# Performance work log

Measured on AMD Instinct MI355X. Metric: run time of the kernel, lower is better.

## Reference

```python
import jax, jax.numpy as jnp
import numpy as np

B, N, D = 64, 1024, 512
H, LD = 8, 64            # num_heads, linear_hidden_dim (H*LD == D)
HIDDEN = 4 * D           # ffn_multiply = 4.0
NB = 128                 # number of timestamp buckets
EPS = 1e-6
TS_SCALE = NB / 14.0     # log1p(1e6) ~ 13.8 -> buckets span [0, NB]


def rms_norm(x, eps=EPS):
    return x * jax.lax.rsqrt(jnp.mean(x * x, axis=-1, keepdims=True) + eps)


def setup_inputs() -> dict:
    key = jax.random.key(0)
    ks = jax.random.split(key, 8)
    lengths = np.linspace(256, N, B).astype(np.int64)
    x_offsets = jnp.asarray(np.concatenate([[0], np.cumsum(lengths)]), dtype=jnp.int64)
    T = int(lengths.sum())
    x = jax.random.normal(ks[0], (T, D), dtype=jnp.float32)
    all_timestamps = jnp.sort(jax.random.randint(ks[1], (B, N), 0, 10**6, dtype=jnp.int64), axis=1)
    invalid_attn_mask = jnp.tril(jnp.ones((N, N), jnp.float32))  # causal
    uv = jax.random.normal(ks[2], (D, 3 * H * LD), dtype=jnp.float32) * 0.02
    pos_w = jax.random.normal(ks[3], (2 * N - 1,), dtype=jnp.float32) * 0.02
    ts_w = jax.random.normal(ks[4], (NB + 1,), dtype=jnp.float32) * 0.02
    w_ams = jax.random.normal(ks[5], (2 * H * LD, D), dtype=jnp.float32) * 0.02
    w1 = jax.random.normal(ks[6], (D, HIDDEN), dtype=jnp.float32) * 0.02
    w2 = jax.random.normal(ks[7], (HIDDEN, D), dtype=jnp.float32) * 0.02
    return {"x": x, "x_offsets": x_offsets, "all_timestamps": all_timestamps,
            "invalid_attn_mask": invalid_attn_mask, "uv": uv, "pos_w": pos_w,
            "ts_w": ts_w, "w_ams": w_ams, "w1": w1, "w2": w2}


def reference(x, x_offsets, all_timestamps, invalid_attn_mask, uv, pos_w, ts_w, w_ams, w1, w2):
    T = x.shape[0]
    # RMSNorm (no learned scale, matches F.rms_norm with no weight) + fused proj + SiLU
    proj = jax.nn.silu(rms_norm(x) @ uv)                       # [T, 3*H*LD]
    u, v = proj[:, :2 * H * LD], proj[:, 2 * H * LD:]          # [T,2HD'], [T,HD']
    # jagged -> padded dense
    tok = jnp.arange(T)
    seg = jnp.searchsorted(x_offsets, tok, side="right") - 1   # batch id per token
    pos = tok - x_offsets[seg]                                  # position within sequence
    padded_v = jnp.zeros((B, N, H * LD), v.dtype).at[seg, pos].set(v).reshape(B, N, H, LD)
    # positional relative bias (batch-independent)
    rel = jnp.arange(N)[:, None] - jnp.arange(N)[None, :]
    pos_attn = pos_w[rel + N - 1] * invalid_attn_mask           # [N,N]
    # temporal relative bias: log-bucketized |t_i - t_j|
    dt = jnp.abs(all_timestamps[:, :, None] - all_timestamps[:, None, :]).astype(jnp.float32)
    bucket = jnp.clip(jnp.floor(jnp.log1p(dt) * TS_SCALE), 0, NB).astype(jnp.int32)
    ts_attn = ts_w[bucket] * invalid_attn_mask[None]            # [B,N,N]
    # two-stream bias 'attention' (no softmax)
    out_pos = jnp.einsum("nm,bmhd->bnhd", pos_attn, padded_v)
    out_ts = jnp.einsum("bnm,bmhd->bnhd", ts_attn, padded_v)
    combined = jnp.concatenate([out_pos, out_ts], axis=-1).reshape(B, N, 2 * H * LD)
    attn_out = combined[seg, pos]                               # dense -> jagged, [T, 2*H*LD]
    # gated norm + multistage FFN with residuals
    ams = u * rms_norm(attn_out)
    h = x + ams @ w_ams
    out = h + jax.nn.silu(rms_norm(h) @ w1) @ w2
    return out
```

## Files before the change

### kernel.cpp

```cpp
#include <hip/hip_runtime.h>
#include <cmath>


using u16 = unsigned short;

typedef __bf16 bf16x8 __attribute__((ext_vector_type(8)));
typedef float  f32x4  __attribute__((ext_vector_type(4)));

#define TS_SCALE_F (float)(128.0 / 14.0)

__device__ __forceinline__ u16 f2b(float f) {
  unsigned u = __float_as_uint(f);
  unsigned r = 0x7FFFu + ((u >> 16) & 1u);
  return (u16)((u + r) >> 16);
}
__device__ __forceinline__ float b2f(u16 v) {
  return __uint_as_float(((unsigned)v) << 16);
}
__device__ __forceinline__ bf16x8 as_frag(uint4 r) {
  union { uint4 u; bf16x8 v; } c; c.u = r; return c.v;
}

__device__ __forceinline__ size_t ts_base_elems(int b, int nt) {
  return (size_t)b * 589824 + (size_t)(nt * (nt + 1) / 2) * 16384;
}

#define EPI_SILU_BF16 0
#define EPI_ADD_F32   1

template <int EPI>
__global__ __launch_bounds__(256, 2) void gemm_bf16(
    const u16* __restrict__ A, const u16* __restrict__ W,
    void* __restrict__ C, const float* __restrict__ ADD,
    int M, int N, int K)
{
  __shared__ u16 lA[128 * 40];
  __shared__ u16 lB[4096];

  const int tid  = threadIdx.x;
  const int t0   = blockIdx.x * 128;
  const int c0   = blockIdx.y * 128;
  const int wave = tid >> 6, lane = tid & 63;
  const int wr   = (wave >> 1) * 64, wc = (wave & 1) * 64;
  const int l15  = lane & 15, l4 = lane >> 4;

  f32x4 z = {0.f, 0.f, 0.f, 0.f};
  f32x4 acc[4][4];
#pragma unroll
  for (int m = 0; m < 4; ++m)
#pragma unroll
    for (int j = 0; j < 4; ++j) acc[m][j] = z;

  const int ar = tid >> 1, ak = (tid & 1) * 16;
  const int bk = tid >> 3, bc = (tid & 7) * 16;
  const bool arow_ok = (t0 + ar) < M;
  const u16* aptr = A + (size_t)(t0 + ar) * K + ak;
  const u16* wptr = W + (size_t)bk * N + c0 + bc;

  for (int k0 = 0; k0 < K; k0 += 32) {
    uint4 a0 = make_uint4(0, 0, 0, 0), a1 = a0;
    if (arow_ok) {
      a0 = *(const uint4*)(aptr + k0);
      a1 = *(const uint4*)(aptr + k0 + 8);
    }
    uint4 w0 = *(const uint4*)(wptr + (size_t)k0 * N);
    uint4 w1v = *(const uint4*)(wptr + (size_t)k0 * N + 8);

    *(uint4*)&lA[ar * 40 + ak]     = a0;
    *(uint4*)&lA[ar * 40 + ak + 8] = a1;
    {
      u16 tmp[16];
      *(uint4*)tmp       = w0;
      *(uint4*)(tmp + 8) = w1v;
      const int kb = bk >> 3, ke = bk & 7;
      char* base = (char*)lB;
#pragma unroll
      for (int i = 0; i < 16; ++i) {
        int col = bc + i;
        int off = (kb * 2048 + col * 16 + ke * 2) ^ (((col >> 3) & 7) << 4);
        *(u16*)(base + off) = tmp[i];
      }
    }
    __syncthreads();

    bf16x8 af[4], bfv[4];
#pragma unroll
    for (int m = 0; m < 4; ++m)
      af[m] = as_frag(*(const uint4*)&lA[(wr + m * 16 + l15) * 40 + l4 * 8]);
#pragma unroll
    for (int j = 0; j < 4; ++j) {
      int col = wc + j * 16 + l15;
      int off = (l4 * 2048 + col * 16) ^ (((col >> 3) & 7) << 4);
      bfv[j] = as_frag(*(const uint4*)((char*)lB + off));
    }
#pragma unroll
    for (int m = 0; m < 4; ++m)
#pragma unroll
      for (int j = 0; j < 4; ++j)
        acc[m][j] = __builtin_amdgcn_mfma_f32_16x16x32_bf16(af[m], bfv[j], acc[m][j], 0, 0, 0);
    __syncthreads();
  }

#pragma unroll
  for (int m = 0; m < 4; ++m) {
#pragma unroll
    for (int r = 0; r < 4; ++r) {
      int row = t0 + wr + m * 16 + l4 * 4 + r;
      if (row >= M) continue;
#pragma unroll
      for (int j = 0; j < 4; ++j) {
        int col = c0 + wc + j * 16 + l15;
        size_t idx = (size_t)row * N + col;
        float y = acc[m][j][r];
        if constexpr (EPI == EPI_SILU_BF16) {
          float s = y / (1.f + __expf(-y));
          ((u16*)C)[idx] = f2b(s);
        } else {
          ((float*)C)[idx] = y + ADD[idx];
        }
      }
    }
  }
}

__global__ __launch_bounds__(128) void pos_scores(
    const float* __restrict__ pos_w, u16* __restrict__ pos_s)
{
  const int n = blockIdx.x;
  const int m0 = threadIdx.x * 8;
  u16 o[8];
#pragma unroll
  for (int i = 0; i < 8; ++i) {
    int m = m0 + i;
    float v = (m <= n) ? pos_w[n - m + 1023] : 0.f;
    o[i] = f2b(v);
  }
  *(uint4*)(pos_s + (size_t)n * 1024 + m0) = *(uint4*)o;
}

__global__ __launch_bounds__(256) void ts_scores(
    const int* __restrict__ tstamp, const float* __restrict__ ts_w,
    u16* __restrict__ ts_s)
{
  const int nt = 7 - (blockIdx.x >> 6);
  const int b  = blockIdx.x & 63;
  const int W  = 128 * (nt + 1);
  const int n0 = nt * 128;
  const int tid = threadIdx.x;

  __shared__ float tsw[132];
  __shared__ int   tsm[1024];
  if (tid < 129) tsw[tid] = ts_w[tid];
  for (int i = tid; i < W; i += 256) tsm[i] = tstamp[b * 1024 + i];
  __syncthreads();

  const int r = tid >> 1, h = tid & 1;
  const int n_abs = n0 + r;
  const int t_n = tstamp[b * 1024 + n_abs];
  u16* row = ts_s + ts_base_elems(b, nt) + (size_t)r * W + h * (W >> 1);
  const int c0 = h * (W >> 1);
  const int half = W >> 1;

  for (int c = 0; c < half; c += 8) {
    u16 o[8];
#pragma unroll
    for (int i = 0; i < 8; ++i) {
      int m = c0 + c + i;
      int d = t_n - tsm[m];
      if (d < 0) d = -d;
      float dt = (float)d;
      int bkt = (int)(log1pf(dt) * TS_SCALE_F);
      bkt = bkt > 128 ? 128 : bkt;
      float v = (m <= n_abs) ? tsw[bkt] : 0.f;
      o[i] = f2b(v);
    }
    *(uint4*)(row + c) = *(uint4*)o;
  }
}

__global__ __launch_bounds__(256, 1) void attn_gemm(
    const u16* __restrict__ proj,
    const int* __restrict__ xoff,
    const u16* __restrict__ pos_s,
    const u16* __restrict__ ts_s,
    u16* __restrict__ attn_out,
    int Ttot)
{
  const int flat = blockIdx.x;
  const int nt = 7 - (flat >> 8);
  const int rem = flat & 255;
  const int b  = rem >> 2;
  const int ct = rem & 3;

  const int off = xoff[b];
  int len = xoff[b + 1] - off;
  if (len < 0) len = 0;
  if (len > 1024) len = 1024;
  if (off < 0 || off + len > Ttot) return;
  const int n0 = nt * 128;
  if (n0 >= len) return;
  const int c0 = ct * 128;
  const int W = 128 * (nt + 1);

  __shared__ u16 lP[128 * 40];
  __shared__ u16 lT[128 * 40];
  __shared__ u16 sV[4096];

  const int tid = threadIdx.x;
  const int wave = tid >> 6, lane = tid & 63;
  const int wr = (wave >> 1) * 64, wc = (wave & 1) * 64;
  const int l15 = lane & 15, l4 = lane >> 4;

  f32x4 z = {0.f, 0.f, 0.f, 0.f};
  f32x4 accP[4][4], accT[4][4];
#pragma unroll
  for (int m = 0; m < 4; ++m)
#pragma unroll
    for (int j = 0; j < 4; ++j) { accP[m][j] = z; accT[m][j] = z; }

  const int ar = tid >> 1, ak = (tid & 1) * 16;
  const u16* pRow = pos_s + (size_t)(n0 + ar) * 1024 + ak;
  const u16* tRow = ts_s + ts_base_elems(b, nt) + (size_t)ar * W + ak;
  const int vk = tid >> 3, vc = (tid & 7) * 16;

  const int mEnd = (n0 + 128 < len) ? (n0 + 128) : len;

  for (int m0 = 0; m0 < mEnd; m0 += 32) {
    {
      int mm = m0 + vk;
      uint4 v0 = make_uint4(0, 0, 0, 0), v1 = v0;
      if (mm < len) {
        const u16* src = proj + (size_t)(off + mm) * 1536 + 1024 + c0 + vc;
        v0 = *(const uint4*)src;
        v1 = *(const uint4*)(src + 8);
      }
      u16 tmp[16];
      *(uint4*)tmp       = v0;
      *(uint4*)(tmp + 8) = v1;
      const int kb = vk >> 3, ke = vk & 7;
#pragma unroll
      for (int i = 0; i < 16; ++i) {
        int col = vc + i;
        int o2 = (kb * 2048 + col * 16 + ke * 2) ^ (((col >> 3) & 7) << 4);
        *(u16*)((char*)sV + o2) = tmp[i];
      }
    }
    {
      uint4 p0 = *(const uint4*)(pRow + m0);
      uint4 p1 = *(const uint4*)(pRow + m0 + 8);
      uint4 t0v = *(const uint4*)(tRow + m0);
      uint4 t1v = *(const uint4*)(tRow + m0 + 8);
      int wb = ar * 40 + ak;
      *(uint4*)&lP[wb]     = p0;
      *(uint4*)&lP[wb + 8] = p1;
      *(uint4*)&lT[wb]     = t0v;
      *(uint4*)&lT[wb + 8] = t1v;
    }
    __syncthreads();

    bf16x8 ap[4], at[4], bv[4];
#pragma unroll
    for (int m = 0; m < 4; ++m) {
      ap[m] = as_frag(*(const uint4*)&lP[(wr + m * 16 + l15) * 40 + l4 * 8]);
      at[m] = as_frag(*(const uint4*)&lT[(wr + m * 16 + l15) * 40 + l4 * 8]);
    }
#pragma unroll
    for (int j = 0; j < 4; ++j) {
      int col = wc + j * 16 + l15;
      int o2 = (l4 * 2048 + col * 16) ^ (((col >> 3) & 7) << 4);
      bv[j] = as_frag(*(const uint4*)((char*)sV + o2));
    }
#pragma unroll
    for (int m = 0; m < 4; ++m)
#pragma unroll
      for (int j = 0; j < 4; ++j) {
        accP[m][j] = __builtin_amdgcn_mfma_f32_16x16x32_bf16(ap[m], bv[j], accP[m][j], 0, 0, 0);
        accT[m][j] = __builtin_amdgcn_mfma_f32_16x16x32_bf16(at[m], bv[j], accT[m][j], 0, 0, 0);
      }
    __syncthreads();
  }

#pragma unroll
  for (int m = 0; m < 4; ++m)
#pragma unroll
    for (int r = 0; r < 4; ++r) {
      int n = n0 + wr + m * 16 + l4 * 4 + r;
      if (n >= len) continue;
      size_t t = (size_t)(off + n);
#pragma unroll
      for (int j = 0; j < 4; ++j) {
        int hd = c0 + wc + j * 16 + l15;
        int colP = ((hd >> 6) << 7) + (hd & 63);
        attn_out[t * 1024 + colP]      = f2b(accP[m][j][r]);
        attn_out[t * 1024 + colP + 64] = f2b(accT[m][j][r]);
      }
    }
}

template <int D, bool HASMUL, bool INBF>
__global__ __launch_bounds__(256) void rms_prep(
    const void* __restrict__ in_, const u16* __restrict__ mul, int mulStride,
    u16* __restrict__ out)
{
  const int row = blockIdx.x;
  const int tid = threadIdx.x;
  const float* rf = (const float*)in_ + (INBF ? 0 : (size_t)row * D);
  const u16*   rb = (const u16*)in_ + (INBF ? (size_t)row * D : 0);
  float ss = 0.f;
#pragma unroll
  for (int i = tid; i < D; i += 256) {
    float v = INBF ? b2f(rb[i]) : rf[i];
    ss += v * v;
  }
#pragma unroll
  for (int o = 32; o > 0; o >>= 1) ss += __shfl_down(ss, o, 64);
  __shared__ float sred[4];
  const int wave = tid >> 6, lane = tid & 63;
  if (lane == 0) sred[wave] = ss;
  __syncthreads();
  float inv = rsqrtf((sred[0] + sred[1] + sred[2] + sred[3]) / (float)D + 1e-6f);
#pragma unroll
  for (int i = tid; i < D; i += 256) {
    float v = (INBF ? b2f(rb[i]) : rf[i]) * inv;
    if constexpr (HASMUL) v *= b2f(mul[(size_t)row * mulStride + i]);
    out[(size_t)row * D + i] = f2b(v);
  }
}

__global__ void cvt_bf16(const float* __restrict__ in, u16* __restrict__ out, int n) {
  int i = blockIdx.x * 256 + threadIdx.x;
  if (i < n) out[i] = f2b(in[i]);
}

extern "C" void kernel_launch(void* const* d_in, const int* in_sizes, int n_in,
                              void* d_out, int out_size, void* d_ws, size_t ws_size,
                              hipStream_t stream)
{
  const float* x      = (const float*)d_in[0];
  const int*   xoff   = (const int*)d_in[1];
  const int*   tstamp = (const int*)d_in[2];
  const float* uv     = (const float*)d_in[4];
  const float* pos_w  = (const float*)d_in[5];
  const float* ts_w   = (const float*)d_in[6];
  const float* w_ams  = (const float*)d_in[7];
  const float* w1     = (const float*)d_in[8];
  const float* w2     = (const float*)d_in[9];
  const int T = in_sizes[0] / 512;

  char* ws = (char*)d_ws;
  size_t o = 0;
  auto take = [&](size_t bytes) { size_t r = o; o += (bytes + 255) & ~(size_t)255; return r; };

  u16* uvb    = (u16*)(ws + take((size_t)512 * 1536 * 2));
  u16* wamsb  = (u16*)(ws + take((size_t)1024 * 512 * 2));
  u16* w1b    = (u16*)(ws + take((size_t)512 * 2048 * 2));
  u16* w2b    = (u16*)(ws + take((size_t)2048 * 512 * 2));
  u16* posS   = (u16*)(ws + take((size_t)1024 * 1024 * 2));

  size_t tsBytes = (size_t)64 * 589824 * 2;
  size_t s2Bytes = (size_t)T * 1024 * 2;
  if (s2Bytes < tsBytes) s2Bytes = tsBytes;
  size_t o_s2 = take(s2Bytes);
  u16* A1   = (u16*)(ws + o_s2);
  u16* tsS  = (u16*)(ws + o_s2);
  u16* A2   = (u16*)(ws + o_s2);
  u16* mid  = (u16*)(ws + o_s2);

  size_t o_proj = take((size_t)T * 1536 * 2);
  u16* proj = (u16*)(ws + o_proj);
  u16* A1p  = proj + (size_t)T * 1024;

  u16*   attnS = (u16*)d_out;
  float* h     = (float*)d_out;

  if (ws_size < o) return;

  cvt_bf16<<<(512 * 1536 + 255) / 256, 256, 0, stream>>>(uv, uvb, 512 * 1536);
  cvt_bf16<<<(1024 * 512 + 255) / 256, 256, 0, stream>>>(w_ams, wamsb, 1024 * 512);
  cvt_bf16<<<(512 * 2048 + 255) / 256, 256, 0, stream>>>(w1, w1b, 512 * 2048);
  cvt_bf16<<<(2048 * 512 + 255) / 256, 256, 0, stream>>>(w2, w2b, 2048 * 512);

  pos_scores<<<1024, 128, 0, stream>>>(pos_w, posS);

  rms_prep<512, false, false><<<T, 256, 0, stream>>>(x, nullptr, 0, A1);

  dim3 g1((T + 127) / 128, 12);
  gemm_bf16<EPI_SILU_BF16><<<g1, 256, 0, stream>>>(A1, uvb, proj, nullptr, T, 1536, 512);

  ts_scores<<<512, 256, 0, stream>>>(tstamp, ts_w, tsS);

  attn_gemm<<<64 * 32, 256, 0, stream>>>(proj, xoff, posS, tsS, attnS, T);

  rms_prep<1024, true, true><<<T, 256, 0, stream>>>(attnS, proj, 1536, A2);

  dim3 g3((T + 127) / 128, 4);
  gemm_bf16<EPI_ADD_F32><<<g3, 256, 0, stream>>>(A2, wamsb, h, x, T, 512, 1024);

  rms_prep<512, false, false><<<T, 256, 0, stream>>>(h, nullptr, 0, A1p);

  dim3 g4((T + 127) / 128, 16);
  gemm_bf16<EPI_SILU_BF16><<<g4, 256, 0, stream>>>(A1p, w1b, mid, nullptr, T, 2048, 512);

  dim3 g5((T + 127) / 128, 4);
  gemm_bf16<EPI_ADD_F32><<<g5, 256, 0, stream>>>(mid, w2b, h, h, T, 512, 2048);
}
```

Baseline: 983.0 us.

## Pre-pack GEMM weights into tile order and load B tiles via global_load_lds

Replaces the flat fp32-to-bf16 weight conversion with a prep kernel that writes the weights in a per-column-panel, per-k-step tiled layout. The GEMM then copies B tiles straight from global memory into LDS with global_load_lds, which removes the per-thread 16-way scalar LDS scatter. The grid is also transposed so that blocks sharing a row tile of A launch next to each other, which should improve A reuse in cache. The new LDS layout drops the XOR swizzle, so B fragment reads may hit more bank conflicts.

```diff
diff --git a/kernel.cpp b/kernel.cpp
--- a/kernel.cpp
+++ b/kernel.cpp
@@ -21,16 +21,40 @@
   union { uint4 u; bf16x8 v; } c; c.u = r; return c.v;
 }
 
+__device__ __forceinline__ void gload_lds16(const u16* g, u16* l) {
+  __builtin_amdgcn_global_load_lds(
+      (const __attribute__((address_space(1))) unsigned int*)g,
+      (__attribute__((address_space(3))) unsigned int*)l, 16, 0, 0);
+}
+
 __device__ __forceinline__ size_t ts_base_elems(int b, int nt) {
   return (size_t)b * 589824 + (size_t)(nt * (nt + 1) / 2) * 16384;
 }
 
+__global__ __launch_bounds__(256) void wprep(
+    const float* __restrict__ W, u16* __restrict__ Wp, int K, int N)
+{
+  const int p = blockIdx.x, s = blockIdx.y;
+  const int t = threadIdx.x;
+  size_t base = ((size_t)p * (K >> 5) + s) * 4096;
+  const int e0 = t * 16;
+  u16 o[16];
+#pragma unroll
+  for (int i = 0; i < 16; ++i) {
+    int e = e0 + i;
+    int kb = e >> 10, r = e & 1023, c = r >> 3, ke = r & 7;
+    o[i] = f2b(W[(size_t)(s * 32 + kb * 8 + ke) * N + p * 128 + c]);
+  }
+  *(uint4*)(Wp + base + e0)     = *(uint4*)o;
+  *(uint4*)(Wp + base + e0 + 8) = *(uint4*)(o + 8);
+}
+
 #define EPI_SILU_BF16 0
 #define EPI_ADD_F32   1
 
 template <int EPI>
 __global__ __launch_bounds__(256, 2) void gemm_bf16(
-    const u16* __restrict__ A, const u16* __restrict__ W,
+    const u16* __restrict__ A, const u16* __restrict__ Wp,
     void* __restrict__ C, const float* __restrict__ ADD,
     int M, int N, int K)
 {
@@ -38,8 +62,9 @@
   __shared__ u16 lB[4096];
 
   const int tid  = threadIdx.x;
-  const int t0   = blockIdx.x * 128;
-  const int c0   = blockIdx.y * 128;
+  const int c0b  = blockIdx.x;
+  const int t0   = blockIdx.y * 128;
+  const int c0   = c0b * 128;
   const int wave = tid >> 6, lane = tid & 63;
   const int wr   = (wave >> 1) * 64, wc = (wave & 1) * 64;
   const int l15  = lane & 15, l4 = lane >> 4;
@@ -52,35 +77,25 @@
     for (int j = 0; j < 4; ++j) acc[m][j] = z;
 
   const int ar = tid >> 1, ak = (tid & 1) * 16;
-  const int bk = tid >> 3, bc = (tid & 7) * 16;
   const bool arow_ok = (t0 + ar) < M;
   const u16* aptr = A + (size_t)(t0 + ar) * K + ak;
-  const u16* wptr = W + (size_t)bk * N + c0 + bc;
-
-  for (int k0 = 0; k0 < K; k0 += 32) {
+  const int ksteps = K >> 5;
+  const u16* wpanel = Wp + (size_t)c0b * ksteps * 4096;
+  const u16* wsrc = wpanel + wave * 1024 + lane * 8;
+  u16* ldsb = &lB[wave * 1024];
+
+  for (int s = 0; s < ksteps; ++s) {
     uint4 a0 = make_uint4(0, 0, 0, 0), a1 = a0;
     if (arow_ok) {
-      a0 = *(const uint4*)(aptr + k0);
-      a1 = *(const uint4*)(aptr + k0 + 8);
-    }
-    uint4 w0 = *(const uint4*)(wptr + (size_t)k0 * N);
-    uint4 w1v = *(const uint4*)(wptr + (size_t)k0 * N + 8);
-
+      a0 = *(const uint4*)(aptr);
+      a1 = *(const uint4*)(aptr + 8);
+    }
+    aptr += 32;
+    gload_lds16(wsrc, ldsb);
+    gload_lds16(wsrc + 512, ldsb + 512);
+    wsrc += 4096;
     *(uint4*)&lA[ar * 40 + ak]     = a0;
     *(uint4*)&lA[ar * 40 + ak + 8] = a1;
-    {
-      u16 tmp[16];
-      *(uint4*)tmp       = w0;
-      *(uint4*)(tmp + 8) = w1v;
-      const int kb = bk >> 3, ke = bk & 7;
-      char* base = (char*)lB;
-#pragma unroll
-      for (int i = 0; i < 16; ++i) {
-        int col = bc + i;
-        int off = (kb * 2048 + col * 16 + ke * 2) ^ (((col >> 3) & 7) << 4);
-        *(u16*)(base + off) = tmp[i];
-      }
-    }
     __syncthreads();
 
     bf16x8 af[4], bfv[4];
@@ -88,11 +103,8 @@
     for (int m = 0; m < 4; ++m)
       af[m] = as_frag(*(const uint4*)&lA[(wr + m * 16 + l15) * 40 + l4 * 8]);
 #pragma unroll
-    for (int j = 0; j < 4; ++j) {
-      int col = wc + j * 16 + l15;
-      int off = (l4 * 2048 + col * 16) ^ (((col >> 3) & 7) << 4);
-      bfv[j] = as_frag(*(const uint4*)((char*)lB + off));
-    }
+    for (int j = 0; j < 4; ++j)
+      bfv[j] = as_frag(*(const uint4*)&lB[(l4 << 10) + (wc + j * 16 + l15) * 8]);
 #pragma unroll
     for (int m = 0; m < 4; ++m)
 #pragma unroll
@@ -327,11 +339,6 @@
   }
 }
 
-__global__ void cvt_bf16(const float* __restrict__ in, u16* __restrict__ out, int n) {
-  int i = blockIdx.x * 256 + threadIdx.x;
-  if (i < n) out[i] = f2b(in[i]);
-}
-
 extern "C" void kernel_launch(void* const* d_in, const int* in_sizes, int n_in,
                               void* d_out, int out_size, void* d_ws, size_t ws_size,
                               hipStream_t stream)
@@ -375,16 +382,16 @@
 
   if (ws_size < o) return;
 
-  cvt_bf16<<<(512 * 1536 + 255) / 256, 256, 0, stream>>>(uv, uvb, 512 * 1536);
-  cvt_bf16<<<(1024 * 512 + 255) / 256, 256, 0, stream>>>(w_ams, wamsb, 1024 * 512);
-  cvt_bf16<<<(512 * 2048 + 255) / 256, 256, 0, stream>>>(w1, w1b, 512 * 2048);
-  cvt_bf16<<<(2048 * 512 + 255) / 256, 256, 0, stream>>>(w2, w2b, 2048 * 512);
+  wprep<<<dim3(12, 16), 256, 0, stream>>>(uv,    uvb,   512,  1536);
+  wprep<<<dim3(4, 32),  256, 0, stream>>>(w_ams, wamsb, 1024, 512);
+  wprep<<<dim3(16, 16), 256, 0, stream>>>(w1,    w1b,   512,  2048);
+  wprep<<<dim3(4, 64),  256, 0, stream>>>(w2,    w2b,   2048, 512);
 
   pos_scores<<<1024, 128, 0, stream>>>(pos_w, posS);
 
   rms_prep<512, false, false><<<T, 256, 0, stream>>>(x, nullptr, 0, A1);
 
-  dim3 g1((T + 127) / 128, 12);
+  dim3 g1(12, (T + 127) / 128);
   gemm_bf16<EPI_SILU_BF16><<<g1, 256, 0, stream>>>(A1, uvb, proj, nullptr, T, 1536, 512);
 
   ts_scores<<<512, 256, 0, stream>>>(tstamp, ts_w, tsS);
@@ -393,14 +400,14 @@
 
   rms_prep<1024, true, true><<<T, 256, 0, stream>>>(attnS, proj, 1536, A2);
 
-  dim3 g3((T + 127) / 128, 4);
+  dim3 g3(4, (T + 127) / 128);
   gemm_bf16<EPI_ADD_F32><<<g3, 256, 0, stream>>>(A2, wamsb, h, x, T, 512, 1024);
 
   rms_prep<512, false, false><<<T, 256, 0, stream>>>(h, nullptr, 0, A1p);
 
-  dim3 g4((T + 127) / 128, 16);
+  dim3 g4(16, (T + 127) / 128);
   gemm_bf16<EPI_SILU_BF16><<<g4, 256, 0, stream>>>(A1p, w1b, mid, nullptr, T, 2048, 512);
 
-  dim3 g5((T + 127) / 128, 4);
+  dim3 g5(4, (T + 127) / 128);
   gemm_bf16<EPI_ADD_F32><<<g5, 256, 0, stream>>>(mid, w2b, h, h, T, 512, 2048);
 }
```

Measured after the change: 939.5 us. 4.4% less time.
